# Optimization experiments

Hardware: AMD Instinct MI355X
Metric: run time of the kernel (lower is better)

## Reference

```python
import jax, jax.numpy as jnp
import numpy as np

B, N, C_IN, C_OUT, E_DIM = 16, 1024, 64, 64, 4


def setup_inputs() -> dict:
    key = jax.random.key(0)
    ks = jax.random.split(key, 7)
    x = jax.random.normal(ks[0], (B, N, C_IN), dtype=jnp.float32)
    adj = jax.random.uniform(ks[1], (B, N, N), dtype=jnp.float32)
    edge_attr = jax.random.randint(ks[2], (B, N, N, 1), 0, E_DIM, dtype=jnp.int32)
    scale = 1.0 / np.sqrt(C_IN)
    W_rel = jax.random.normal(ks[3], (C_IN, C_OUT), dtype=jnp.float32) * scale
    b_rel = jax.random.normal(ks[4], (C_OUT,), dtype=jnp.float32) * scale
    W_root = jax.random.normal(ks[5], (C_IN, C_OUT), dtype=jnp.float32) * scale
    w_edge = jax.random.normal(ks[6], (E_DIM,), dtype=jnp.float32)
    return {"x": x, "adj": adj, "edge_attr": edge_attr,
            "W_rel": W_rel, "b_rel": b_rel, "W_root": W_root, "w_edge": w_edge}


def reference(x, adj, edge_attr, W_rel, b_rel, W_root, w_edge):
    # one_hot(edge_attr) @ w_edge == gather of w_edge by edge type (same math,
    # avoids materializing the B x N x N x E_DIM one-hot tensor).
    e = w_edge[edge_attr[..., 0]]            # [B, N, N]
    adj_w = adj * e                           # weighted adjacency
    out = jnp.matmul(adj_w, x)                # [B, N, C_IN] aggregation (aggr='add')
    out = jnp.matmul(out, W_rel) + b_rel      # lin_rel
    out = out + jnp.matmul(x, W_root)         # lin_root (no bias)
    return out
```

## Files before the change

### kernel.cpp

```cpp
#include <hip/hip_runtime.h>

#define BB 16
#define NN 1024
#define CC 64

typedef __attribute__((ext_vector_type(8))) short short8;
typedef __attribute__((ext_vector_type(4))) float f32x4;

__device__ __forceinline__ unsigned short bf16_rne(float f) {
    unsigned u = __float_as_uint(f);
    u += 0x7fffu + ((u >> 16) & 1u);
    return (unsigned short)(u >> 16);
}

extern "C" __global__ __launch_bounds__(256)
void precompute(const float* __restrict__ x, const float* __restrict__ W_rel,
                const float* __restrict__ W_root, const float* __restrict__ b_rel,
                unsigned short* __restrict__ xw_sw, float* __restrict__ out)
{
    __shared__ float wrel_s[64 * 64];
    __shared__ float wroot_s[64 * 64];
    __shared__ float x_s[16 * 68];

    const int t = threadIdx.x;
    #pragma unroll
    for (int k = 0; k < 4; ++k) {
        int i4 = t + 256 * k;
        ((float4*)wrel_s)[i4]  = ((const float4*)W_rel)[i4];
        ((float4*)wroot_s)[i4] = ((const float4*)W_root)[i4];
    }
    const int row0 = blockIdx.x * 16;
    {
        int r = t >> 4, c4 = t & 15;
        *(float4*)(x_s + r * 68 + c4 * 4) = ((const float4*)(x + (size_t)(row0 + r) * CC))[c4];
    }
    __syncthreads();

    const int c4 = t & 15;
    const int r  = t >> 4;
    float aw0 = 0.f, aw1 = 0.f, aw2 = 0.f, aw3 = 0.f;
    float ar0 = 0.f, ar1 = 0.f, ar2 = 0.f, ar3 = 0.f;
    const float* xrow = x_s + r * 68;
    #pragma unroll 8
    for (int k = 0; k < 64; ++k) {
        float xv = xrow[k];
        float4 wv = ((const float4*)(wrel_s  + k * 64))[c4];
        float4 rv = ((const float4*)(wroot_s + k * 64))[c4];
        aw0 += xv * wv.x; aw1 += xv * wv.y; aw2 += xv * wv.z; aw3 += xv * wv.w;
        ar0 += xv * rv.x; ar1 += xv * rv.y; ar2 += xv * rv.z; ar3 += xv * rv.w;
    }

    const int row_g = row0 + r;
    {
        const float4 bv = ((const float4*)b_rel)[c4];
        ((float4*)out)[(size_t)row_g * 16 + c4] =
            make_float4(ar0 + bv.x, ar1 + bv.y, ar2 + bv.z, ar3 + bv.w);
    }
    {
        const int b = row_g >> 10;
        const int k = row_g & 1023;
        const int kb = k >> 5;
        const int qk = (k >> 3) & 3;
        const int j  = k & 7;
        const int c  = 4 * c4;
        const int n0 = c >> 4;
        const int n  = c & 15;
        size_t off = ((size_t)b << 16) + (size_t)((kb * 4 + n0) << 9)
                   + (size_t)((n + (qk << 4)) << 3) + j;
        xw_sw[off]      = bf16_rne(aw0);
        xw_sw[off + 8]  = bf16_rne(aw1);
        xw_sw[off + 16] = bf16_rne(aw2);
        xw_sw[off + 24] = bf16_rne(aw3);
    }
}

extern "C" __global__ __launch_bounds__(256, 4)
void gnn_mfma(const float* __restrict__ adj, const int* __restrict__ ea,
              const float* __restrict__ w_edge,
              const unsigned short* __restrict__ xw_sw,
              float* __restrict__ out)
{
    __shared__ float red_s[3 * 16 * 64];

    const int t    = threadIdx.x;
    const int w    = t >> 6;
    const int lane = t & 63;
    const int m    = lane & 15;
    const int q    = lane >> 4;
    const int b     = blockIdx.x >> 6;
    const int mtile = blockIdx.x & 63;

    const float w0 = w_edge[0], w1 = w_edge[1], w2 = w_edge[2], w3 = w_edge[3];
    const float d1 = w1 - w0;
    const float d2 = w2 - 2.f * w1 + w0;
    const float d3 = w3 - 3.f * w2 + 3.f * w1 - w0;
    const float c3 = d3 * (1.f / 6.f);
    const float c2 = 0.5f * d2 - 0.5f * d3;
    const float c1 = d1 - 0.5f * d2 + (1.f / 3.f) * d3;
    const float c0 = w0;

    const int row = (mtile << 4) + m;
    const float* arow = adj + (((size_t)b << 10) + row) * NN + (w << 8) + (q << 3);
    const int*   erow = ea  + (((size_t)b << 10) + row) * NN + (w << 8) + (q << 3);
    const short8* xf  = (const short8*)(xw_sw + ((size_t)b << 16) + (w << 14)) + lane;

    f32x4 acc0 = {0.f, 0.f, 0.f, 0.f};
    f32x4 acc1 = acc0, acc2 = acc0, acc3 = acc0;

    #pragma unroll 2
    for (int kk = 0; kk < 8; ++kk) {
        const float* ap = arow + (kk << 5);
        const int*   ep = erow + (kk << 5);
        float4 a0 = *(const float4*)ap;
        float4 a1 = *(const float4*)(ap + 4);
        int4   e0 = *(const int4*)ep;
        int4   e1 = *(const int4*)(ep + 4);

        #define WSEL(e) __builtin_fmaf(__builtin_fmaf(__builtin_fmaf(c3, (float)(e), c2), (float)(e), c1), (float)(e), c0)
        float p0 = a0.x * WSEL(e0.x);
        float p1 = a0.y * WSEL(e0.y);
        float p2 = a0.z * WSEL(e0.z);
        float p3 = a0.w * WSEL(e0.w);
        float p4 = a1.x * WSEL(e1.x);
        float p5 = a1.y * WSEL(e1.y);
        float p6 = a1.z * WSEL(e1.z);
        float p7 = a1.w * WSEL(e1.w);
        #undef WSEL

        union { int i[4]; short8 s; } af;
        af.i[0] = __builtin_amdgcn_perm(__float_as_uint(p1), __float_as_uint(p0), 0x07060302u);
        af.i[1] = __builtin_amdgcn_perm(__float_as_uint(p3), __float_as_uint(p2), 0x07060302u);
        af.i[2] = __builtin_amdgcn_perm(__float_as_uint(p5), __float_as_uint(p4), 0x07060302u);
        af.i[3] = __builtin_amdgcn_perm(__float_as_uint(p7), __float_as_uint(p6), 0x07060302u);

        short8 bf0 = xf[(kk * 4 + 0) * 64];
        short8 bf1 = xf[(kk * 4 + 1) * 64];
        short8 bf2 = xf[(kk * 4 + 2) * 64];
        short8 bf3 = xf[(kk * 4 + 3) * 64];

        acc0 = __builtin_amdgcn_mfma_f32_16x16x32_bf16(af.s, bf0, acc0, 0, 0, 0);
        acc1 = __builtin_amdgcn_mfma_f32_16x16x32_bf16(af.s, bf1, acc1, 0, 0, 0);
        acc2 = __builtin_amdgcn_mfma_f32_16x16x32_bf16(af.s, bf2, acc2, 0, 0, 0);
        acc3 = __builtin_amdgcn_mfma_f32_16x16x32_bf16(af.s, bf3, acc3, 0, 0, 0);
    }

    if (w != 0) {
        float* buf = red_s + (w - 1) * 1024;
        #pragma unroll
        for (int rg = 0; rg < 4; ++rg) {
            int rbase = (q * 4 + rg) * 64 + m;
            buf[rbase]      = acc0[rg];
            buf[rbase + 16] = acc1[rg];
            buf[rbase + 32] = acc2[rg];
            buf[rbase + 48] = acc3[rg];
        }
    }
    __syncthreads();
    if (w == 0) {
        float* obase = out + (((size_t)b << 10) + (mtile << 4)) * 64;
        #pragma unroll
        for (int rg = 0; rg < 4; ++rg) {
            int rbase = (q * 4 + rg) * 64 + m;
            #pragma unroll
            for (int n0 = 0; n0 < 4; ++n0) {
                int idx = rbase + n0 * 16;
                float v = (n0 == 0 ? acc0[rg] : n0 == 1 ? acc1[rg] : n0 == 2 ? acc2[rg] : acc3[rg]);
                v += red_s[idx] + red_s[1024 + idx] + red_s[2048 + idx];
                obase[idx] += v;
            }
        }
    }
}

extern "C" void kernel_launch(void* const* d_in, const int* in_sizes, int n_in,
                              void* d_out, int out_size, void* d_ws, size_t ws_size,
                              hipStream_t stream) {
    const float* x      = (const float*)d_in[0];
    const float* adj    = (const float*)d_in[1];
    const int*   ea     = (const int*)  d_in[2];
    const float* W_rel  = (const float*)d_in[3];
    const float* b_rel  = (const float*)d_in[4];
    const float* W_root = (const float*)d_in[5];
    const float* w_edge = (const float*)d_in[6];
    float* out = (float*)d_out;

    unsigned short* xw_sw = (unsigned short*)d_ws;

    precompute<<<BB * NN / 16, 256, 0, stream>>>(x, W_rel, W_root, b_rel, xw_sw, out);
    gnn_mfma<<<BB * (NN / 16), 256, 0, stream>>>(adj, ea, w_edge, xw_sw, out);
}
```

Before: 178.2 us.

## Hoist all adj/edge loads upfront and double-buffer B fragments in gnn_mfma

Each wave now issues all eight iterations' adjacency and edge-attribute loads before the compute loop, behind a scheduling barrier. Inside the fully unrolled loop it prefetches the next iteration's bf16 B fragments. This is meant to expose more memory-level parallelism on the bandwidth-bound adj/ea stream. It raises register pressure, so the launch-bounds occupancy hint drops from 4 to 2, and the reduction buffer in shared memory is padded to 68 floats per row to reduce bank conflicts.

Measured after the change: 176.0 us. Within noise of the previous version (-1.3%).

```diff
diff --git a/kernel.cpp b/kernel.cpp
--- a/kernel.cpp
+++ b/kernel.cpp
@@ -74,13 +74,13 @@
     }
 }
 
-extern "C" __global__ __launch_bounds__(256, 4)
+extern "C" __global__ __launch_bounds__(256, 2)
 void gnn_mfma(const float* __restrict__ adj, const int* __restrict__ ea,
               const float* __restrict__ w_edge,
               const unsigned short* __restrict__ xw_sw,
               float* __restrict__ out)
 {
-    __shared__ float red_s[3 * 16 * 64];
+    __shared__ float red_s[3 * 1088];
 
     const int t    = threadIdx.x;
     const int w    = t >> 6;
@@ -100,23 +100,42 @@
     const float c0 = w0;
 
     const int row = (mtile << 4) + m;
-    const float* arow = adj + (((size_t)b << 10) + row) * NN + (w << 8) + (q << 3);
-    const int*   erow = ea  + (((size_t)b << 10) + row) * NN + (w << 8) + (q << 3);
-    const short8* xf  = (const short8*)(xw_sw + ((size_t)b << 16) + (w << 14)) + lane;
+    const size_t rowoff = (((size_t)b << 10) + row) * NN + (w << 8) + (q << 3);
+    const float* arow = adj + rowoff;
+    const int*   erow = ea  + rowoff;
+    const short8* xf  = (const short8*)(xw_sw + ((size_t)b << 16)) + lane;
+
+    float4 a[8][2];
+    int4   e[8][2];
+    #pragma unroll
+    for (int kk = 0; kk < 8; ++kk) {
+        a[kk][0] = *(const float4*)(arow + (kk << 5));
+        a[kk][1] = *(const float4*)(arow + (kk << 5) + 4);
+        e[kk][0] = *(const int4*)  (erow + (kk << 5));
+        e[kk][1] = *(const int4*)  (erow + (kk << 5) + 4);
+    }
+    short8 bf0 = xf[((w * 8 + 0) * 4 + 0) * 64];
+    short8 bf1 = xf[((w * 8 + 0) * 4 + 1) * 64];
+    short8 bf2 = xf[((w * 8 + 0) * 4 + 2) * 64];
+    short8 bf3 = xf[((w * 8 + 0) * 4 + 3) * 64];
+    __builtin_amdgcn_sched_barrier(0);
 
     f32x4 acc0 = {0.f, 0.f, 0.f, 0.f};
     f32x4 acc1 = acc0, acc2 = acc0, acc3 = acc0;
 
-    #pragma unroll 2
+    #pragma unroll
     for (int kk = 0; kk < 8; ++kk) {
-        const float* ap = arow + (kk << 5);
-        const int*   ep = erow + (kk << 5);
-        float4 a0 = *(const float4*)ap;
-        float4 a1 = *(const float4*)(ap + 4);
-        int4   e0 = *(const int4*)ep;
-        int4   e1 = *(const int4*)(ep + 4);
-
-        #define WSEL(e) __builtin_fmaf(__builtin_fmaf(__builtin_fmaf(c3, (float)(e), c2), (float)(e), c1), (float)(e), c0)
+        short8 nb0, nb1, nb2, nb3;
+        if (kk < 7) {
+            nb0 = xf[((w * 8 + kk + 1) * 4 + 0) * 64];
+            nb1 = xf[((w * 8 + kk + 1) * 4 + 1) * 64];
+            nb2 = xf[((w * 8 + kk + 1) * 4 + 2) * 64];
+            nb3 = xf[((w * 8 + kk + 1) * 4 + 3) * 64];
+        }
+        float4 a0 = a[kk][0], a1 = a[kk][1];
+        int4   e0 = e[kk][0], e1 = e[kk][1];
+
+        #define WSEL(ev) __builtin_fmaf(__builtin_fmaf(__builtin_fmaf(c3, (float)(ev), c2), (float)(ev), c1), (float)(ev), c0)
         float p0 = a0.x * WSEL(e0.x);
         float p1 = a0.y * WSEL(e0.y);
         float p2 = a0.z * WSEL(e0.z);
@@ -133,22 +152,19 @@
         af.i[2] = __builtin_amdgcn_perm(__float_as_uint(p5), __float_as_uint(p4), 0x07060302u);
         af.i[3] = __builtin_amdgcn_perm(__float_as_uint(p7), __float_as_uint(p6), 0x07060302u);
 
-        short8 bf0 = xf[(kk * 4 + 0) * 64];
-        short8 bf1 = xf[(kk * 4 + 1) * 64];
-        short8 bf2 = xf[(kk * 4 + 2) * 64];
-        short8 bf3 = xf[(kk * 4 + 3) * 64];
-
         acc0 = __builtin_amdgcn_mfma_f32_16x16x32_bf16(af.s, bf0, acc0, 0, 0, 0);
         acc1 = __builtin_amdgcn_mfma_f32_16x16x32_bf16(af.s, bf1, acc1, 0, 0, 0);
         acc2 = __builtin_amdgcn_mfma_f32_16x16x32_bf16(af.s, bf2, acc2, 0, 0, 0);
         acc3 = __builtin_amdgcn_mfma_f32_16x16x32_bf16(af.s, bf3, acc3, 0, 0, 0);
+
+        if (kk < 7) { bf0 = nb0; bf1 = nb1; bf2 = nb2; bf3 = nb3; }
     }
 
     if (w != 0) {
-        float* buf = red_s + (w - 1) * 1024;
+        float* buf = red_s + (w - 1) * 1088;
         #pragma unroll
         for (int rg = 0; rg < 4; ++rg) {
-            int rbase = (q * 4 + rg) * 64 + m;
+            int rbase = (q * 4 + rg) * 68 + m;
             buf[rbase]      = acc0[rg];
             buf[rbase + 16] = acc1[rg];
             buf[rbase + 32] = acc2[rg];
@@ -160,13 +176,14 @@
         float* obase = out + (((size_t)b << 10) + (mtile << 4)) * 64;
         #pragma unroll
         for (int rg = 0; rg < 4; ++rg) {
-            int rbase = (q * 4 + rg) * 64 + m;
+            int rpad = (q * 4 + rg) * 68 + m;
+            int rout = (q * 4 + rg) * 64 + m;
             #pragma unroll
             for (int n0 = 0; n0 < 4; ++n0) {
-                int idx = rbase + n0 * 16;
+                int idx  = rpad + n0 * 16;
                 float v = (n0 == 0 ? acc0[rg] : n0 == 1 ? acc1[rg] : n0 == 2 ? acc2[rg] : acc3[rg]);
-                v += red_s[idx] + red_s[1024 + idx] + red_s[2048 + idx];
-                obase[idx] += v;
+                v += red_s[idx] + red_s[1088 + idx] + red_s[2176 + idx];
+                obase[rout + n0 * 16] += v;
             }
         }
     }
```

## Split K dimension across two blocks with atomic accumulation into output

Applied to the files above, without the earlier changes.

Doubles the grid by splitting each row tile's 1024-long reduction into two halves handled by separate blocks, which then combine results with atomicAdd into the output. The loop is fully unrolled with the B-fragment loads hoisted ahead of the adjacency math, launch bounds are raised to 6 blocks per CU, and the shared reduction buffer is padded to a row stride of 68 to avoid bank conflicts. The goal is more memory-level parallelism and occupancy for this bandwidth-bound kernel. In exchange it adds float atomics, which make the summation order nondeterministic, and doubles the reduction epilogue work.

Result: no change. 175.6 us (-1.5%).

```diff
diff --git a/kernel.cpp b/kernel.cpp
--- a/kernel.cpp
+++ b/kernel.cpp
@@ -74,21 +74,23 @@
     }
 }
 
-extern "C" __global__ __launch_bounds__(256, 4)
+extern "C" __global__ __launch_bounds__(256, 6)
 void gnn_mfma(const float* __restrict__ adj, const int* __restrict__ ea,
               const float* __restrict__ w_edge,
               const unsigned short* __restrict__ xw_sw,
               float* __restrict__ out)
 {
-    __shared__ float red_s[3 * 16 * 64];
+    __shared__ float red_s[3 * 1088];
 
     const int t    = threadIdx.x;
     const int w    = t >> 6;
     const int lane = t & 63;
     const int m    = lane & 15;
     const int q    = lane >> 4;
-    const int b     = blockIdx.x >> 6;
+
     const int mtile = blockIdx.x & 63;
+    const int khalf = (blockIdx.x >> 6) & 1;
+    const int b     = blockIdx.x >> 7;
 
     const float w0 = w_edge[0], w1 = w_edge[1], w2 = w_edge[2], w3 = w_edge[3];
     const float d1 = w1 - w0;
@@ -100,23 +102,29 @@
     const float c0 = w0;
 
     const int row = (mtile << 4) + m;
-    const float* arow = adj + (((size_t)b << 10) + row) * NN + (w << 8) + (q << 3);
-    const int*   erow = ea  + (((size_t)b << 10) + row) * NN + (w << 8) + (q << 3);
-    const short8* xf  = (const short8*)(xw_sw + ((size_t)b << 16) + (w << 14)) + lane;
+    const size_t rowoff = (((size_t)b << 10) + row) * NN + (khalf << 9) + (w << 7) + (q << 3);
+    const float* arow = adj + rowoff;
+    const int*   erow = ea  + rowoff;
+    const int kb0 = (khalf << 4) + (w << 2);
+    const short8* xf = (const short8*)(xw_sw + ((size_t)b << 16)) + lane;
 
     f32x4 acc0 = {0.f, 0.f, 0.f, 0.f};
     f32x4 acc1 = acc0, acc2 = acc0, acc3 = acc0;
 
-    #pragma unroll 2
-    for (int kk = 0; kk < 8; ++kk) {
+    #pragma unroll
+    for (int kk = 0; kk < 4; ++kk) {
         const float* ap = arow + (kk << 5);
         const int*   ep = erow + (kk << 5);
         float4 a0 = *(const float4*)ap;
         float4 a1 = *(const float4*)(ap + 4);
         int4   e0 = *(const int4*)ep;
         int4   e1 = *(const int4*)(ep + 4);
+        short8 bf0 = xf[((kb0 + kk) * 4 + 0) * 64];
+        short8 bf1 = xf[((kb0 + kk) * 4 + 1) * 64];
+        short8 bf2 = xf[((kb0 + kk) * 4 + 2) * 64];
+        short8 bf3 = xf[((kb0 + kk) * 4 + 3) * 64];
 
-        #define WSEL(e) __builtin_fmaf(__builtin_fmaf(__builtin_fmaf(c3, (float)(e), c2), (float)(e), c1), (float)(e), c0)
+        #define WSEL(ev) __builtin_fmaf(__builtin_fmaf(__builtin_fmaf(c3, (float)(ev), c2), (float)(ev), c1), (float)(ev), c0)
         float p0 = a0.x * WSEL(e0.x);
         float p1 = a0.y * WSEL(e0.y);
         float p2 = a0.z * WSEL(e0.z);
@@ -133,11 +141,6 @@
         af.i[2] = __builtin_amdgcn_perm(__float_as_uint(p5), __float_as_uint(p4), 0x07060302u);
         af.i[3] = __builtin_amdgcn_perm(__float_as_uint(p7), __float_as_uint(p6), 0x07060302u);
 
-        short8 bf0 = xf[(kk * 4 + 0) * 64];
-        short8 bf1 = xf[(kk * 4 + 1) * 64];
-        short8 bf2 = xf[(kk * 4 + 2) * 64];
-        short8 bf3 = xf[(kk * 4 + 3) * 64];
-
         acc0 = __builtin_amdgcn_mfma_f32_16x16x32_bf16(af.s, bf0, acc0, 0, 0, 0);
         acc1 = __builtin_amdgcn_mfma_f32_16x16x32_bf16(af.s, bf1, acc1, 0, 0, 0);
         acc2 = __builtin_amdgcn_mfma_f32_16x16x32_bf16(af.s, bf2, acc2, 0, 0, 0);
@@ -145,10 +148,10 @@
     }
 
     if (w != 0) {
-        float* buf = red_s + (w - 1) * 1024;
+        float* buf = red_s + (w - 1) * 1088;
         #pragma unroll
         for (int rg = 0; rg < 4; ++rg) {
-            int rbase = (q * 4 + rg) * 64 + m;
+            int rbase = (q * 4 + rg) * 68 + m;
             buf[rbase]      = acc0[rg];
             buf[rbase + 16] = acc1[rg];
             buf[rbase + 32] = acc2[rg];
@@ -160,13 +163,14 @@
         float* obase = out + (((size_t)b << 10) + (mtile << 4)) * 64;
         #pragma unroll
         for (int rg = 0; rg < 4; ++rg) {
-            int rbase = (q * 4 + rg) * 64 + m;
+            int rpad = (q * 4 + rg) * 68 + m;
+            int rout = (q * 4 + rg) * 64 + m;
             #pragma unroll
             for (int n0 = 0; n0 < 4; ++n0) {
-                int idx = rbase + n0 * 16;
+                int idx = rpad + n0 * 16;
                 float v = (n0 == 0 ? acc0[rg] : n0 == 1 ? acc1[rg] : n0 == 2 ? acc2[rg] : acc3[rg]);
-                v += red_s[idx] + red_s[1024 + idx] + red_s[2048 + idx];
-                obase[idx] += v;
+                v += red_s[idx] + red_s[1088 + idx] + red_s[2176 + idx];
+                atomicAdd(obase + rout + n0 * 16, v);
             }
         }
     }
@@ -187,5 +191,5 @@
     unsigned short* xw_sw = (unsigned short*)d_ws;
 
     precompute<<<BB * NN / 16, 256, 0, stream>>>(x, W_rel, W_root, b_rel, xw_sw, out);
-    gnn_mfma<<<BB * (NN / 16), 256, 0, stream>>>(adj, ea, w_edge, xw_sw, out);
+    gnn_mfma<<<BB * (NN / 16) * 2, 256, 0, stream>>>(adj, ea, w_edge, xw_sw, out);
 }
```
